# Kernel optimization log

Hardware: AMD Instinct MI355X
Metric: run time of the kernel (lower is better)

Reference implementation:

```python
import jax, jax.numpy as jnp
import numpy as np
from jax import lax

COCO_80_TO_91 = [1,2,3,4,5,6,7,8,9,10,11,13,14,15,16,17,18,19,20,21,22,23,24,25,27,28,31,32,33,34,35,36,37,38,39,40,41,42,43,44,46,47,48,49,50,51,52,53,54,55,56,57,58,59,60,61,62,63,64,65,67,70,72,73,74,75,76,77,78,79,80,81,82,84,85,86,87,88,89,90]

CONF = 0.25      # self.confidence
IOU_THR = 0.7    # ultralytics NMS default
TOPK = 1000      # candidate cap before NMS
MAX_DET = 300    # ultralytics max_det default
MAX_WH = 7680.0  # per-class offset trick
IMG_SZ = 640.0   # yolov8 letterboxed input size


def setup_inputs() -> dict:
    key = jax.random.key(0)
    preds = jax.random.uniform(key, (32, 84, 8400), dtype=jnp.float32)
    return {"preds": preds}


def _nms_single(boxes, scores):
    """Greedy NMS on score-descending boxes [K,4] (class-offset xyxy). Returns keep mask [K]."""
    K = boxes.shape[0]
    area = (boxes[:, 2] - boxes[:, 0]) * (boxes[:, 3] - boxes[:, 1])  # [K]
    lt = jnp.maximum(boxes[:, None, :2], boxes[None, :, :2])          # [K,K,2]
    rb = jnp.minimum(boxes[:, None, 2:], boxes[None, :, 2:])
    wh = jnp.clip(rb - lt, 0.0)
    inter = wh[..., 0] * wh[..., 1]
    iou = inter / (area[:, None] + area[None, :] - inter + 1e-7)       # [K,K]
    idx = jnp.arange(K)
    sup = (iou > IOU_THR) & (idx[None, :] > idx[:, None])              # i suppresses later j

    def body(i, keep):
        return jnp.where(keep[i], keep & ~sup[i], keep)

    return lax.fori_loop(0, K, body, jnp.ones((K,), dtype=bool))


def reference(preds):
    # preds: [B, 84, N] -> [B, N, 84]
    p = jnp.transpose(preds, (0, 2, 1))
    box_xywh = p[..., :4] * IMG_SZ           # xywh in pixels on 640x640 canvas
    cls = p[..., 4:]                          # [B, N, 80]
    scores = jnp.max(cls, axis=-1)            # best-class confidence
    labels = jnp.argmax(cls, axis=-1)         # 0..79
    xy, wh = box_xywh[..., :2], box_xywh[..., 2:]
    xyxy = jnp.concatenate([xy - wh * 0.5, xy + wh * 0.5], axis=-1)  # decode

    # confidence filter + top-K candidate selection (score-descending)
    s_masked = jnp.where(scores > CONF, scores, -1.0)
    top_s, top_i = lax.top_k(s_masked, TOPK)                          # [B,TOPK]
    top_b = jnp.take_along_axis(xyxy, top_i[..., None], axis=1)      # [B,TOPK,4]
    top_l = jnp.take_along_axis(labels, top_i, axis=1)               # [B,TOPK]

    # per-class NMS via class offset
    off_b = top_b + (top_l.astype(top_b.dtype) * MAX_WH)[..., None]
    keep = jax.vmap(_nms_single)(off_b, top_s) & (top_s > CONF)

    # select final max_det detections, zero-pad invalid slots
    fin_s = jnp.where(keep, top_s, -1.0)
    out_s, out_i = lax.top_k(fin_s, MAX_DET)                          # [B,MAX_DET]
    out_b = jnp.take_along_axis(top_b, out_i[..., None], axis=1)
    out_l = jnp.take_along_axis(top_l, out_i, axis=1)
    valid = out_s > CONF
    boxes = jnp.where(valid[..., None], out_b, 0.0)
    scores_out = jnp.where(valid, out_s, 0.0)
    mapped = jnp.asarray(COCO_80_TO_91, dtype=jnp.int64)[out_l]       # COCO 80 -> 91 ids
    labels_out = jnp.where(valid, mapped, 0)
    return boxes, scores_out, labels_out
```

## Files before the change

kernel.cpp:

```cpp
#include <hip/hip_runtime.h>
#include <stdint.h>

typedef unsigned long long u64;
typedef unsigned int u32;

#define BATCH 32
#define NCH 84
#define NA 8400
#define NCLS 80
#define TOPK 1000
#define MAXDET 300
#define CONF 0.25f
#define IOU_T 0.7f
#define MAX_WH 7680.0f
#define IMG_SZ 640.0f
#define NT 1024
#define KPT 9
#define NCOPY 8
#define HPAD 260
#define DTILE 256

__device__ __constant__ float coco_map_f[NCLS] = {
    1,2,3,4,5,6,7,8,9,10,11,13,14,15,16,17,18,19,20,21,22,23,24,25,27,28,
    31,32,33,34,35,36,37,38,39,40,41,42,43,44,46,47,48,49,50,51,52,53,54,
    55,56,57,58,59,60,61,62,63,64,65,67,70,72,73,74,75,76,77,78,79,80,81,
    82,84,85,86,87,88,89,90};

__device__ inline u64 shflx64(u64 v, int m) {
    int lo = __shfl_xor((int)(u32)(v & 0xFFFFFFFFull), m, 64);
    int hi = __shfl_xor((int)(u32)(v >> 32), m, 64);
    return ((u64)(u32)hi << 32) | (u32)lo;
}

__global__ __launch_bounds__(256)
void decode_kernel(const float* __restrict__ preds,
                   u64* __restrict__ keys,
                   float4* __restrict__ boxes) {
    const int b = blockIdx.y;
    const int a_base = blockIdx.x * DTILE;
    const int t = threadIdx.x;
    const int a = a_base + t;
    const float* p = preds + (size_t)b * NCH * NA;

    __shared__ float stage[16][DTILE];

    float bx = 0.f, by = 0.f, bw = 0.f, bh = 0.f;
    float best = -1.0f;
    int bl = 0;

    for (int chunk = 0; chunk < 6; ++chunk) {
        const int r0 = chunk * 16;
        const int nr = (chunk == 5) ? 4 : 16;
        if (chunk) __syncthreads();
        for (int i = 0; i < nr / 4; ++i) {
            int idx = i * 256 + t;
            int rl = idx >> 6;
            int c4 = (idx & 63) * 4;
            int col = a_base + c4;
            float4 v = (col < NA) ? *(const float4*)(p + (size_t)(r0 + rl) * NA + col)
                                  : make_float4(0.f, 0.f, 0.f, 0.f);
            *(float4*)&stage[rl][c4] = v;
        }
        __syncthreads();
        if (chunk == 0) {
            bx = stage[0][t]; by = stage[1][t];
            bw = stage[2][t]; bh = stage[3][t];
            best = stage[4][t]; bl = 0;
            for (int r = 5; r < 16; ++r) {
                float v = stage[r][t];
                int c = r - 4;
                bl = (v > best) ? c : bl;  best = fmaxf(v, best);
            }
        } else {
            for (int r = 0; r < nr; ++r) {
                float v = stage[r][t];
                int c = r0 + r - 4;
                bl = (v > best) ? c : bl;  best = fmaxf(v, best);
            }
        }
    }

    if (a < NA) {
        float fx = bx * IMG_SZ, fy = by * IMG_SZ;
        float fw = bw * IMG_SZ, fh = bh * IMG_SZ;
        float hw = fw * 0.5f, hh = fh * 0.5f;
        boxes[(size_t)b * NA + a] = make_float4(fx - hw, fy - hh, fx + hw, fy + hh);
        float s = (best > CONF) ? best : -1.0f;
        u32 fb = __float_as_uint(s);
        u32 u = (fb & 0x80000000u) ? ~fb : (fb | 0x80000000u);
        keys[(size_t)b * NA + a] =
            ((u64)u << 21) | ((u64)(16383 - a) << 7) | (u64)bl;
    }
}

__global__ __launch_bounds__(NT)
void fused_kernel(const u64* __restrict__ keys,
                  const float4* __restrict__ boxes,
                  float* __restrict__ out) {
    const int b = blockIdx.x;
    const int t = threadIdx.x;
    const int lane = t & 63, wid = t >> 6;

    __shared__ union {
        struct {
            u64 sk[2][NT];
            int hist[NCOPY * HPAD];
        } a;
        struct {
            u64 cmask2[NCLS][16];
        } bb;
        struct {
            float4 obox[NT];
            float  area[NT];
            unsigned short ranks[NCLS][64];
            int    cnt[NCLS];
            unsigned char cls[NT];
            unsigned char keep[NT];
        } c;
    } u_s;
    __shared__ int selB, selK, hselS, smax, scnt, cnt_s;
    __shared__ int wsum[16], woff[16], ktot_s;

    u64 kreg[KPT];
    const u64* kb = keys + (size_t)b * NA;
    int nk = 0;
    for (int i = t; i < NA; i += NT) kreg[nk++] = kb[i];

    u64 P = 0ull;
    int kk = TOPK;
    int nsel = 0;
    for (int d = 6; d >= 0; --d) {
        __syncthreads();
        if (t == 0) { smax = -1; scnt = 0; }
        __syncthreads();
        u64 hmask = (~0ull) << (8 * (d + 1));
        int dig[KPT];
        int mymax = -1;
#pragma unroll
        for (int i = 0; i < KPT; ++i) {
            bool act = (i < nk) && (((kreg[i] ^ P) & hmask) == 0ull);
            dig[i] = act ? (int)((kreg[i] >> (8 * d)) & 255) : -1;
            mymax = max(mymax, dig[i]);
        }
#pragma unroll
        for (int off = 32; off; off >>= 1)
            mymax = max(mymax, __shfl_down(mymax, off, 64));
        if (lane == 0) atomicMax(&smax, mymax);
        __syncthreads();
        int maxb = smax;
        int myc = 0;
#pragma unroll
        for (int i = 0; i < KPT; ++i) myc += (dig[i] == maxb) ? 1 : 0;
#pragma unroll
        for (int off = 32; off; off >>= 1) myc += __shfl_down(myc, off, 64);
        if (lane == 0) atomicAdd(&scnt, myc);
        __syncthreads();
        int cm = scnt;
        if (cm >= kk) {
            P |= ((u64)maxb) << (8 * d);
            nsel = TOPK - kk + cm;
            if (nsel <= NT) break;
            continue;
        }
        for (int i = t; i < NCOPY * HPAD; i += NT) u_s.a.hist[i] = 0;
        __syncthreads();
        int* myh = u_s.a.hist + (wid & (NCOPY - 1)) * HPAD;
#pragma unroll
        for (int i = 0; i < KPT; ++i)
            if (dig[i] >= 0) atomicAdd(&myh[dig[i]], 1);
        __syncthreads();
        if (t < 64) {
            int h0 = 0, h1 = 0, h2 = 0, h3 = 0;
            for (int c = 0; c < NCOPY; ++c) {
                const int* hp = u_s.a.hist + c * HPAD + 4 * t;
                h0 += hp[0]; h1 += hp[1]; h2 += hp[2]; h3 += hp[3];
            }
            int s = h0 + h1 + h2 + h3;
            int S = s;
            #pragma unroll
            for (int off = 1; off < 64; off <<= 1) {
                int o = __shfl_down(S, off, 64);
                if (t + off < 64) S += o;
            }
            int Snext = S - s;
            int c3 = Snext + h3, c2 = c3 + h2, c1 = c2 + h1, c0 = c1 + h0;
            int cand = -1, above = 0;
            if (c0 >= kk) {
                if      (c3 >= kk) { cand = 4 * t + 3; above = Snext; }
                else if (c2 >= kk) { cand = 4 * t + 2; above = c3; }
                else if (c1 >= kk) { cand = 4 * t + 1; above = c2; }
                else               { cand = 4 * t;     above = c1; }
            }
            int pc = (cand < 0) ? 0 : (((cand + 1) << 16) | (kk - above));
            #pragma unroll
            for (int off = 32; off; off >>= 1)
                pc = max(pc, __shfl_down(pc, off, 64));
            pc = __shfl(pc, 0, 64);
            int B = (pc >> 16) - 1;
            if (t == (B >> 2)) {
                int m4 = B & 3;
                selB = B;
                selK = pc & 0xFFFF;
                hselS = (m4 == 0) ? h0 : (m4 == 1) ? h1 : (m4 == 2) ? h2 : h3;
            }
        }
        __syncthreads();
        P |= ((u64)selB) << (8 * d);
        kk = selK;
        nsel = TOPK - kk + hselS;
        if (nsel <= NT) break;
    }

    __syncthreads();
    if (t == 0) cnt_s = 0;
    __syncthreads();
    for (int i = 0; i < KPT; ++i) {
        bool p = (i < nk) && (kreg[i] >= P);
        u64 m = __ballot(p);
        int base = 0;
        if (lane == 0) base = atomicAdd(&cnt_s, (int)__popcll(m));
        base = __shfl(base, 0, 64);
        if (p) u_s.a.sk[0][base + (int)__popcll(m & ((1ull << lane) - 1ull))] = kreg[i];
    }
    if (t < NT - nsel) u_s.a.sk[0][nsel + t] = 0ull;
    __syncthreads();

    u64 myk = u_s.a.sk[0][t];
    int buf = 1;
    for (int size = 2; size <= NT; size <<= 1) {
        bool up = ((t & size) == 0);
        for (int stride = size >> 1; stride; stride >>= 1) {
            u64 pk;
            if (stride >= 64) {
                u_s.a.sk[buf][t] = myk;
                __syncthreads();
                pk = u_s.a.sk[buf][t ^ stride];
                buf ^= 1;
            } else {
                pk = shflx64(myk, stride);
            }
            bool tlow = ((t & stride) == 0);
            u64 mn = (myk < pk) ? myk : pk;
            u64 mx = (myk < pk) ? pk : myk;
            myk = up ? (tlow ? mx : mn) : (tlow ? mn : mx);
        }
    }

    __syncthreads();
    for (int i = t; i < NCLS * 16; i += NT) ((u64*)u_s.bb.cmask2)[i] = 0ull;
    __syncthreads();

    int my_L = 0;
    float sj = -1.0f;
    float4 bx = make_float4(0.f, 0.f, 0.f, 0.f);
    if (t < TOPK) {
        int my_a = 16383 - (int)((myk >> 7) & 16383ull);
        my_L = (int)(myk & 127ull);
        bx = boxes[(size_t)b * NA + my_a];
        u32 u = (u32)(myk >> 21);
        u32 fb = (u & 0x80000000u) ? (u ^ 0x80000000u) : ~u;
        sj = __uint_as_float(fb);
        atomicOr(&u_s.bb.cmask2[my_L][t >> 6], 1ull << (t & 63));
    }
    __syncthreads();
    int r = 0, cntreg = 0;
    if (t < TOPK) {
        int w = t >> 6;
        r = __popcll(u_s.bb.cmask2[my_L][w] & ((1ull << (t & 63)) - 1ull));
        for (int q = 0; q < w; ++q) r += __popcll(u_s.bb.cmask2[my_L][q]);
    }
    if (t < NCLS) {
#pragma unroll
        for (int q = 0; q < 16; ++q) cntreg += __popcll(u_s.bb.cmask2[t][q]);
    }
    __syncthreads();

    float off = (float)my_L * MAX_WH;
    float ox0 = bx.x + off, oy0 = bx.y + off, ox1 = bx.z + off, oy1 = bx.w + off;
    float ar = (ox1 - ox0) * (oy1 - oy0);
    if (t < TOPK) {
        u_s.c.obox[t] = make_float4(ox0, oy0, ox1, oy1);
        u_s.c.area[t] = ar;
        u_s.c.cls[t]  = (unsigned char)my_L;
        if (r < 64) u_s.c.ranks[my_L][r] = (unsigned short)t;
    } else {
        u_s.c.cls[t] = 255;
    }
    u_s.c.keep[t] = 0;
    if (t < NCLS) u_s.c.cnt[t] = cntreg;
    __syncthreads();

    for (int cc = wid; cc < NCLS; cc += 16) {
        int n = u_s.c.cnt[cc];
        if (n == 0) continue;
        if (n <= 64) {
            float4 bbx = make_float4(0.f, 0.f, 0.f, 0.f);
            float aa = 0.f;
            int rk = 0;
            if (lane < n) {
                rk  = u_s.c.ranks[cc][lane];
                bbx = u_s.c.obox[rk];
                aa  = u_s.c.area[rk];
            }
            u64 colm = 0ull;
            for (int i = 0; i < n; ++i) {
                float hx0 = __shfl(bbx.x, i, 64);
                float hy0 = __shfl(bbx.y, i, 64);
                float hx1 = __shfl(bbx.z, i, 64);
                float hy1 = __shfl(bbx.w, i, 64);
                float ha  = __shfl(aa, i, 64);
                float lx = fmaxf(hx0, bbx.x), ly = fmaxf(hy0, bbx.y);
                float rx = fminf(hx1, bbx.z), ry = fminf(hy1, bbx.w);
                float w = fmaxf(rx - lx, 0.0f);
                float h = fmaxf(ry - ly, 0.0f);
                float inter = w * h;
                float denom = ha + aa;
                denom = denom - inter;
                denom = denom + 1e-7f;
                bool s = (lane > i) && (lane < n) && (inter / denom > IOU_T);
                colm |= ((u64)s) << i;
            }
            u64 alive = (n >= 64) ? ~0ull : ((1ull << n) - 1ull);
            for (int i = 0; i < n; ++i) {
                if (!((alive >> i) & 1ull)) continue;
                alive &= ~__ballot((colm >> i) & 1ull);
            }
            if (lane < n) u_s.c.keep[rk] = (unsigned char)((alive >> lane) & 1ull);
        } else if (lane == 0) {
            u64 aliveW[16];
            for (int q = 0; q < 16; ++q) aliveW[q] = ~0ull;
            for (int i = 0; i < TOPK; ++i) {
                if (u_s.c.cls[i] != (unsigned char)cc) continue;
                if (!((aliveW[i >> 6] >> (i & 63)) & 1ull)) continue;
                float4 bi = u_s.c.obox[i];
                float ai = u_s.c.area[i];
                for (int j = i + 1; j < TOPK; ++j) {
                    if (u_s.c.cls[j] != (unsigned char)cc) continue;
                    if (!((aliveW[j >> 6] >> (j & 63)) & 1ull)) continue;
                    float4 bj = u_s.c.obox[j];
                    float lx = fmaxf(bi.x, bj.x), ly = fmaxf(bi.y, bj.y);
                    float rx = fminf(bi.z, bj.z), ry = fminf(bi.w, bj.w);
                    float w = fmaxf(rx - lx, 0.0f);
                    float h = fmaxf(ry - ly, 0.0f);
                    float inter = w * h;
                    float denom = ai + u_s.c.area[j];
                    denom = denom - inter;
                    denom = denom + 1e-7f;
                    if (inter / denom > IOU_T) aliveW[j >> 6] &= ~(1ull << (j & 63));
                }
            }
            for (int i = 0; i < TOPK; ++i)
                if (u_s.c.cls[i] == (unsigned char)cc)
                    u_s.c.keep[i] = (unsigned char)((aliveW[i >> 6] >> (i & 63)) & 1ull);
        }
    }
    __syncthreads();

    bool valid = (t < TOPK) && u_s.c.keep[t] && (sj > CONF);
    u64 m = __ballot(valid);
    if (lane == 0) wsum[wid] = (int)__popcll(m);
    __syncthreads();
    if (wid == 0) {
        int v = (lane < 16) ? wsum[lane] : 0;
        #pragma unroll
        for (int o = 1; o < 16; o <<= 1) {
            int x = __shfl_up(v, o, 64);
            if (lane >= o) v += x;
        }
        if (lane < 16) woff[lane] = v - wsum[lane];
        if (lane == 15) ktot_s = v;
    }
    __syncthreads();
    int ktot = ktot_s;
    int rank = woff[wid] + (int)__popcll(m & ((1ull << lane) - 1ull));

    float* out_boxes = out;
    float* out_scores = out + (size_t)BATCH * MAXDET * 4;
    float* out_labels = out + (size_t)BATCH * MAXDET * 5;
    if (valid && rank < MAXDET) {
        float* ob = out_boxes + ((size_t)b * MAXDET + rank) * 4;
        ob[0] = bx.x; ob[1] = bx.y; ob[2] = bx.z; ob[3] = bx.w;
        out_scores[(size_t)b * MAXDET + rank] = sj;
        out_labels[(size_t)b * MAXDET + rank] = coco_map_f[my_L];
    }
    if (t < MAXDET && t >= ktot) {
        float* ob = out_boxes + ((size_t)b * MAXDET + t) * 4;
        ob[0] = 0.0f; ob[1] = 0.0f; ob[2] = 0.0f; ob[3] = 0.0f;
        out_scores[(size_t)b * MAXDET + t] = 0.0f;
        out_labels[(size_t)b * MAXDET + t] = 0.0f;
    }
}

extern "C" void kernel_launch(void* const* d_in, const int* in_sizes, int n_in,
                              void* d_out, int out_size, void* d_ws, size_t ws_size,
                              hipStream_t stream) {
    const float* preds = (const float*)d_in[0];
    char* ws = (char*)d_ws;
    size_t off = 0;
    auto alloc = [&](size_t bytes) { char* p = ws + off; off += (bytes + 255) & ~(size_t)255; return p; };

    u64* keys     = (u64*)    alloc((size_t)BATCH * NA * 8);
    float4* boxes = (float4*) alloc((size_t)BATCH * NA * 16);
    float* out = (float*)d_out;

    dim3 dgrid((NA + DTILE - 1) / DTILE, BATCH);
    decode_kernel<<<dgrid, 256, 0, stream>>>(preds, keys, boxes);
    fused_kernel<<<BATCH, NT, 0, stream>>>(keys, boxes, out);
}
```

Before: 189.4 us.

## Split fused select/NMS kernel, skip low radix digits, use per-wave decode staging

The decode kernel now has each wave stage its own 64 columns in shared memory and sync with s_waitcnt instead of block-wide barriers. The radix select only walks the four score digits, since the low key bits are anchor index and label and never matter for score ties at the top-k boundary. The single fused kernel is split into a select+sort kernel that writes sorted keys, boxes, per-class ranks and counts to global memory, and an NMS/epilogue kernel that reads them back. The split cuts shared-memory use per kernel but adds a launch and global round-trips, and the large-class fallback now reads from global memory.

Result: faster. 184.1 us (-2.8%).

```diff
diff --git a/kernel.cpp b/kernel.cpp
--- a/kernel.cpp
+++ b/kernel.cpp
@@ -37,47 +37,50 @@
                    u64* __restrict__ keys,
                    float4* __restrict__ boxes) {
     const int b = blockIdx.y;
-    const int a_base = blockIdx.x * DTILE;
     const int t = threadIdx.x;
-    const int a = a_base + t;
+    const int w = t >> 6, l = t & 63;
+    const int wa = blockIdx.x * DTILE + w * 64;
+    const int a = wa + l;
     const float* p = preds + (size_t)b * NCH * NA;
 
-    __shared__ float stage[16][DTILE];
+    __shared__ float stage[4][16][64];
 
     float bx = 0.f, by = 0.f, bw = 0.f, bh = 0.f;
     float best = -1.0f;
     int bl = 0;
 
+    const int rsel = l >> 4;
+    const int c4 = (l & 15) * 4;
+    const int col = wa + c4;
+
     for (int chunk = 0; chunk < 6; ++chunk) {
         const int r0 = chunk * 16;
+        const int nq = (chunk == 5) ? 1 : 4;
+        for (int i = 0; i < nq; ++i) {
+            int row = r0 + i * 4 + rsel;
+            float4 v = (col < NA) ? *(const float4*)(p + (size_t)row * NA + col)
+                                  : make_float4(0.f, 0.f, 0.f, 0.f);
+            *(float4*)&stage[w][i * 4 + rsel][c4] = v;
+        }
+        __builtin_amdgcn_s_waitcnt(0xc07f);
         const int nr = (chunk == 5) ? 4 : 16;
-        if (chunk) __syncthreads();
-        for (int i = 0; i < nr / 4; ++i) {
-            int idx = i * 256 + t;
-            int rl = idx >> 6;
-            int c4 = (idx & 63) * 4;
-            int col = a_base + c4;
-            float4 v = (col < NA) ? *(const float4*)(p + (size_t)(r0 + rl) * NA + col)
-                                  : make_float4(0.f, 0.f, 0.f, 0.f);
-            *(float4*)&stage[rl][c4] = v;
-        }
-        __syncthreads();
         if (chunk == 0) {
-            bx = stage[0][t]; by = stage[1][t];
-            bw = stage[2][t]; bh = stage[3][t];
-            best = stage[4][t]; bl = 0;
+            bx = stage[w][0][l]; by = stage[w][1][l];
+            bw = stage[w][2][l]; bh = stage[w][3][l];
+            best = stage[w][4][l]; bl = 0;
             for (int r = 5; r < 16; ++r) {
-                float v = stage[r][t];
+                float v = stage[w][r][l];
                 int c = r - 4;
                 bl = (v > best) ? c : bl;  best = fmaxf(v, best);
             }
         } else {
             for (int r = 0; r < nr; ++r) {
-                float v = stage[r][t];
+                float v = stage[w][r][l];
                 int c = r0 + r - 4;
                 bl = (v > best) ? c : bl;  best = fmaxf(v, best);
             }
         }
+        __builtin_amdgcn_s_waitcnt(0xc07f);
     }
 
     if (a < NA) {
@@ -94,9 +97,12 @@
 }
 
 __global__ __launch_bounds__(NT)
-void fused_kernel(const u64* __restrict__ keys,
-                  const float4* __restrict__ boxes,
-                  float* __restrict__ out) {
+void select_sort_kernel(const u64* __restrict__ keys,
+                        const float4* __restrict__ boxes,
+                        u64* __restrict__ sortedk,
+                        float4* __restrict__ gbox,
+                        unsigned short* __restrict__ grank,
+                        int* __restrict__ gccnt) {
     const int b = blockIdx.x;
     const int t = threadIdx.x;
     const int lane = t & 63, wid = t >> 6;
@@ -109,17 +115,8 @@
         struct {
             u64 cmask2[NCLS][16];
         } bb;
-        struct {
-            float4 obox[NT];
-            float  area[NT];
-            unsigned short ranks[NCLS][64];
-            int    cnt[NCLS];
-            unsigned char cls[NT];
-            unsigned char keep[NT];
-        } c;
     } u_s;
     __shared__ int selB, selK, hselS, smax, scnt, cnt_s;
-    __shared__ int wsum[16], woff[16], ktot_s;
 
     u64 kreg[KPT];
     const u64* kb = keys + (size_t)b * NA;
@@ -129,17 +126,18 @@
     u64 P = 0ull;
     int kk = TOPK;
     int nsel = 0;
-    for (int d = 6; d >= 0; --d) {
+    for (int d = 3; d >= 0; --d) {
+        const int sh = 21 + 8 * d;
         __syncthreads();
         if (t == 0) { smax = -1; scnt = 0; }
         __syncthreads();
-        u64 hmask = (~0ull) << (8 * (d + 1));
+        u64 hmask = (~0ull) << (sh + 8);
         int dig[KPT];
         int mymax = -1;
 #pragma unroll
         for (int i = 0; i < KPT; ++i) {
             bool act = (i < nk) && (((kreg[i] ^ P) & hmask) == 0ull);
-            dig[i] = act ? (int)((kreg[i] >> (8 * d)) & 255) : -1;
+            dig[i] = act ? (int)((kreg[i] >> sh) & 255) : -1;
             mymax = max(mymax, dig[i]);
         }
 #pragma unroll
@@ -157,7 +155,7 @@
         __syncthreads();
         int cm = scnt;
         if (cm >= kk) {
-            P |= ((u64)maxb) << (8 * d);
+            P |= ((u64)maxb) << sh;
             nsel = TOPK - kk + cm;
             if (nsel <= NT) break;
             continue;
@@ -205,7 +203,7 @@
             }
         }
         __syncthreads();
-        P |= ((u64)selB) << (8 * d);
+        P |= ((u64)selB) << sh;
         kk = selK;
         nsel = TOPK - kk + hselS;
         if (nsel <= NT) break;
@@ -220,7 +218,10 @@
         int base = 0;
         if (lane == 0) base = atomicAdd(&cnt_s, (int)__popcll(m));
         base = __shfl(base, 0, 64);
-        if (p) u_s.a.sk[0][base + (int)__popcll(m & ((1ull << lane) - 1ull))] = kreg[i];
+        if (p) {
+            int pos = base + (int)__popcll(m & ((1ull << lane) - 1ull));
+            if (pos < NT) u_s.a.sk[0][pos] = kreg[i];
+        }
     }
     if (t < NT - nsel) u_s.a.sk[0][nsel + t] = 0ull;
     __syncthreads();
@@ -245,62 +246,73 @@
             myk = up ? (tlow ? mx : mn) : (tlow ? mn : mx);
         }
     }
+    sortedk[(size_t)b * NT + t] = myk;
 
     __syncthreads();
     for (int i = t; i < NCLS * 16; i += NT) ((u64*)u_s.bb.cmask2)[i] = 0ull;
     __syncthreads();
 
     int my_L = 0;
-    float sj = -1.0f;
     float4 bx = make_float4(0.f, 0.f, 0.f, 0.f);
     if (t < TOPK) {
         int my_a = 16383 - (int)((myk >> 7) & 16383ull);
         my_L = (int)(myk & 127ull);
         bx = boxes[(size_t)b * NA + my_a];
-        u32 u = (u32)(myk >> 21);
-        u32 fb = (u & 0x80000000u) ? (u ^ 0x80000000u) : ~u;
-        sj = __uint_as_float(fb);
         atomicOr(&u_s.bb.cmask2[my_L][t >> 6], 1ull << (t & 63));
     }
     __syncthreads();
-    int r = 0, cntreg = 0;
     if (t < TOPK) {
         int w = t >> 6;
-        r = __popcll(u_s.bb.cmask2[my_L][w] & ((1ull << (t & 63)) - 1ull));
+        int r = __popcll(u_s.bb.cmask2[my_L][w] & ((1ull << (t & 63)) - 1ull));
         for (int q = 0; q < w; ++q) r += __popcll(u_s.bb.cmask2[my_L][q]);
+        gbox[(size_t)b * NT + t] = bx;
+        if (r < 64) grank[((size_t)b * NCLS + my_L) * 64 + r] = (unsigned short)t;
     }
     if (t < NCLS) {
-#pragma unroll
-        for (int q = 0; q < 16; ++q) cntreg += __popcll(u_s.bb.cmask2[t][q]);
-    }
-    __syncthreads();
-
-    float off = (float)my_L * MAX_WH;
-    float ox0 = bx.x + off, oy0 = bx.y + off, ox1 = bx.z + off, oy1 = bx.w + off;
-    float ar = (ox1 - ox0) * (oy1 - oy0);
-    if (t < TOPK) {
-        u_s.c.obox[t] = make_float4(ox0, oy0, ox1, oy1);
-        u_s.c.area[t] = ar;
-        u_s.c.cls[t]  = (unsigned char)my_L;
-        if (r < 64) u_s.c.ranks[my_L][r] = (unsigned short)t;
-    } else {
-        u_s.c.cls[t] = 255;
-    }
-    u_s.c.keep[t] = 0;
-    if (t < NCLS) u_s.c.cnt[t] = cntreg;
-    __syncthreads();
-
-    for (int cc = wid; cc < NCLS; cc += 16) {
-        int n = u_s.c.cnt[cc];
+        int s = 0;
+#pragma unroll
+        for (int q = 0; q < 16; ++q) s += __popcll(u_s.bb.cmask2[t][q]);
+        gccnt[(size_t)b * NCLS + t] = s;
+    }
+}
+
+__global__ __launch_bounds__(NT)
+void nms_epi_kernel(const u64* __restrict__ sortedk,
+                    const float4* __restrict__ gbox,
+                    const unsigned short* __restrict__ grank,
+                    const int* __restrict__ gccnt,
+                    float* __restrict__ out) {
+    const int b = blockIdx.x;
+    const int t = threadIdx.x;
+    const int lane = t & 63, wid = t >> 6;
+
+    __shared__ unsigned char keep[NT];
+    __shared__ int wsum[16], woff[16], ktot_s;
+
+    keep[t] = 0;
+
+    int cnts[5];
+#pragma unroll
+    for (int j = 0; j < 5; ++j)
+        cnts[j] = gccnt[(size_t)b * NCLS + wid + 16 * j];
+
+    u64 myk = sortedk[(size_t)b * NT + t];
+    __syncthreads();
+
+    for (int j = 0; j < 5; ++j) {
+        const int cc = wid + 16 * j;
+        const int n = cnts[j];
         if (n == 0) continue;
         if (n <= 64) {
             float4 bbx = make_float4(0.f, 0.f, 0.f, 0.f);
             float aa = 0.f;
             int rk = 0;
             if (lane < n) {
-                rk  = u_s.c.ranks[cc][lane];
-                bbx = u_s.c.obox[rk];
-                aa  = u_s.c.area[rk];
+                rk = grank[((size_t)b * NCLS + cc) * 64 + lane];
+                float4 g = gbox[(size_t)b * NT + rk];
+                float off = (float)cc * MAX_WH;
+                bbx = make_float4(g.x + off, g.y + off, g.z + off, g.w + off);
+                aa = (bbx.z - bbx.x) * (bbx.w - bbx.y);
             }
             u64 colm = 0ull;
             for (int i = 0; i < n; ++i) {
@@ -325,38 +337,53 @@
                 if (!((alive >> i) & 1ull)) continue;
                 alive &= ~__ballot((colm >> i) & 1ull);
             }
-            if (lane < n) u_s.c.keep[rk] = (unsigned char)((alive >> lane) & 1ull);
+            if (lane < n) keep[rk] = (unsigned char)((alive >> lane) & 1ull);
         } else if (lane == 0) {
+            const u64* skb = sortedk + (size_t)b * NT;
+            const float4* gb = gbox + (size_t)b * NT;
+            const float off = (float)cc * MAX_WH;
             u64 aliveW[16];
             for (int q = 0; q < 16; ++q) aliveW[q] = ~0ull;
             for (int i = 0; i < TOPK; ++i) {
-                if (u_s.c.cls[i] != (unsigned char)cc) continue;
+                if ((int)(skb[i] & 127ull) != cc) continue;
                 if (!((aliveW[i >> 6] >> (i & 63)) & 1ull)) continue;
-                float4 bi = u_s.c.obox[i];
-                float ai = u_s.c.area[i];
-                for (int j = i + 1; j < TOPK; ++j) {
-                    if (u_s.c.cls[j] != (unsigned char)cc) continue;
-                    if (!((aliveW[j >> 6] >> (j & 63)) & 1ull)) continue;
-                    float4 bj = u_s.c.obox[j];
-                    float lx = fmaxf(bi.x, bj.x), ly = fmaxf(bi.y, bj.y);
-                    float rx = fminf(bi.z, bj.z), ry = fminf(bi.w, bj.w);
-                    float w = fmaxf(rx - lx, 0.0f);
-                    float h = fmaxf(ry - ly, 0.0f);
-                    float inter = w * h;
-                    float denom = ai + u_s.c.area[j];
+                float4 g = gb[i];
+                float ix0 = g.x + off, iy0 = g.y + off;
+                float ix1 = g.z + off, iy1 = g.w + off;
+                float ai = (ix1 - ix0) * (iy1 - iy0);
+                for (int jj = i + 1; jj < TOPK; ++jj) {
+                    if ((int)(skb[jj] & 127ull) != cc) continue;
+                    if (!((aliveW[jj >> 6] >> (jj & 63)) & 1ull)) continue;
+                    float4 h = gb[jj];
+                    float jx0 = h.x + off, jy0 = h.y + off;
+                    float jx1 = h.z + off, jy1 = h.w + off;
+                    float aj = (jx1 - jx0) * (jy1 - jy0);
+                    float lx = fmaxf(ix0, jx0), ly = fmaxf(iy0, jy0);
+                    float rx = fminf(ix1, jx1), ry = fminf(iy1, jy1);
+                    float ww = fmaxf(rx - lx, 0.0f);
+                    float hh = fmaxf(ry - ly, 0.0f);
+                    float inter = ww * hh;
+                    float denom = ai + aj;
                     denom = denom - inter;
                     denom = denom + 1e-7f;
-                    if (inter / denom > IOU_T) aliveW[j >> 6] &= ~(1ull << (j & 63));
+                    if (inter / denom > IOU_T) aliveW[jj >> 6] &= ~(1ull << (jj & 63));
                 }
             }
             for (int i = 0; i < TOPK; ++i)
-                if (u_s.c.cls[i] == (unsigned char)cc)
-                    u_s.c.keep[i] = (unsigned char)((aliveW[i >> 6] >> (i & 63)) & 1ull);
-        }
-    }
-    __syncthreads();
-
-    bool valid = (t < TOPK) && u_s.c.keep[t] && (sj > CONF);
+                if ((int)(skb[i] & 127ull) == cc)
+                    keep[i] = (unsigned char)((aliveW[i >> 6] >> (i & 63)) & 1ull);
+        }
+    }
+    __syncthreads();
+
+    float sj = 0.0f;
+    bool valid = false;
+    if (t < TOPK) {
+        u32 u = (u32)(myk >> 21);
+        u32 fb = (u & 0x80000000u) ? (u ^ 0x80000000u) : ~u;
+        sj = __uint_as_float(fb);
+        valid = keep[t] && (sj > CONF);
+    }
     u64 m = __ballot(valid);
     if (lane == 0) wsum[wid] = (int)__popcll(m);
     __syncthreads();
@@ -378,10 +405,11 @@
     float* out_scores = out + (size_t)BATCH * MAXDET * 4;
     float* out_labels = out + (size_t)BATCH * MAXDET * 5;
     if (valid && rank < MAXDET) {
+        float4 bx = gbox[(size_t)b * NT + t];
         float* ob = out_boxes + ((size_t)b * MAXDET + rank) * 4;
         ob[0] = bx.x; ob[1] = bx.y; ob[2] = bx.z; ob[3] = bx.w;
         out_scores[(size_t)b * MAXDET + rank] = sj;
-        out_labels[(size_t)b * MAXDET + rank] = coco_map_f[my_L];
+        out_labels[(size_t)b * MAXDET + rank] = coco_map_f[(int)(myk & 127ull)];
     }
     if (t < MAXDET && t >= ktot) {
         float* ob = out_boxes + ((size_t)b * MAXDET + t) * 4;
@@ -399,11 +427,17 @@
     size_t off = 0;
     auto alloc = [&](size_t bytes) { char* p = ws + off; off += (bytes + 255) & ~(size_t)255; return p; };
 
-    u64* keys     = (u64*)    alloc((size_t)BATCH * NA * 8);
-    float4* boxes = (float4*) alloc((size_t)BATCH * NA * 16);
+    u64* keys            = (u64*)           alloc((size_t)BATCH * NA * 8);
+    float4* boxes        = (float4*)        alloc((size_t)BATCH * NA * 16);
+    u64* sortedk         = (u64*)           alloc((size_t)BATCH * NT * 8);
+    float4* gbox         = (float4*)        alloc((size_t)BATCH * NT * 16);
+    unsigned short* grank= (unsigned short*)alloc((size_t)BATCH * NCLS * 64 * 2);
+    int* gccnt           = (int*)           alloc((size_t)BATCH * NCLS * 4);
     float* out = (float*)d_out;
 
     dim3 dgrid((NA + DTILE - 1) / DTILE, BATCH);
     decode_kernel<<<dgrid, 256, 0, stream>>>(preds, keys, boxes);
-    fused_kernel<<<BATCH, NT, 0, stream>>>(keys, boxes, out);
+    select_sort_kernel<<<BATCH, NT, 0, stream>>>(keys, boxes, sortedk,
+                                                 gbox, grank, gccnt);
+    nms_epi_kernel<<<BATCH, NT, 0, stream>>>(sortedk, gbox, grank, gccnt, out);
 }
```

## Use per-wave staging in decode and shorten radix select to score digits

Applied to the files above, without the earlier changes.

The decode kernel now stages its rows per wavefront, so each wave loads and reads only its own slice. This replaces the block-wide __syncthreads with s_waitcnt. The top-K radix select now starts at the score bits of the packed key, running four 8-bit passes from bit 21 upward instead of seven passes from bit 0. Key loading is fully unrolled with zero-fill, and a bound check guards the candidate scatter. Dropping the low index bits from the select could change which candidates are kept when scores tie, and relying on waitcnt without a barrier assumes LDS accesses within a wave are ordered.

New measurement: 176.3 us. 6.9% less time.

```diff
diff --git a/kernel.cpp b/kernel.cpp
--- a/kernel.cpp
+++ b/kernel.cpp
@@ -37,47 +37,50 @@
                    u64* __restrict__ keys,
                    float4* __restrict__ boxes) {
     const int b = blockIdx.y;
-    const int a_base = blockIdx.x * DTILE;
     const int t = threadIdx.x;
-    const int a = a_base + t;
+    const int w = t >> 6, l = t & 63;
+    const int wa = blockIdx.x * DTILE + w * 64;
+    const int a = wa + l;
     const float* p = preds + (size_t)b * NCH * NA;
 
-    __shared__ float stage[16][DTILE];
+    __shared__ float stage[4][16][64];
 
     float bx = 0.f, by = 0.f, bw = 0.f, bh = 0.f;
     float best = -1.0f;
     int bl = 0;
 
+    const int rsel = l >> 4;
+    const int c4 = (l & 15) * 4;
+    const int col = wa + c4;
+
     for (int chunk = 0; chunk < 6; ++chunk) {
         const int r0 = chunk * 16;
+        const int nq = (chunk == 5) ? 1 : 4;
+        for (int i = 0; i < nq; ++i) {
+            int row = r0 + i * 4 + rsel;
+            float4 v = (col < NA) ? *(const float4*)(p + (size_t)row * NA + col)
+                                  : make_float4(0.f, 0.f, 0.f, 0.f);
+            *(float4*)&stage[w][i * 4 + rsel][c4] = v;
+        }
+        __builtin_amdgcn_s_waitcnt(0xc07f);
         const int nr = (chunk == 5) ? 4 : 16;
-        if (chunk) __syncthreads();
-        for (int i = 0; i < nr / 4; ++i) {
-            int idx = i * 256 + t;
-            int rl = idx >> 6;
-            int c4 = (idx & 63) * 4;
-            int col = a_base + c4;
-            float4 v = (col < NA) ? *(const float4*)(p + (size_t)(r0 + rl) * NA + col)
-                                  : make_float4(0.f, 0.f, 0.f, 0.f);
-            *(float4*)&stage[rl][c4] = v;
-        }
-        __syncthreads();
         if (chunk == 0) {
-            bx = stage[0][t]; by = stage[1][t];
-            bw = stage[2][t]; bh = stage[3][t];
-            best = stage[4][t]; bl = 0;
+            bx = stage[w][0][l]; by = stage[w][1][l];
+            bw = stage[w][2][l]; bh = stage[w][3][l];
+            best = stage[w][4][l]; bl = 0;
             for (int r = 5; r < 16; ++r) {
-                float v = stage[r][t];
+                float v = stage[w][r][l];
                 int c = r - 4;
                 bl = (v > best) ? c : bl;  best = fmaxf(v, best);
             }
         } else {
             for (int r = 0; r < nr; ++r) {
-                float v = stage[r][t];
+                float v = stage[w][r][l];
                 int c = r0 + r - 4;
                 bl = (v > best) ? c : bl;  best = fmaxf(v, best);
             }
         }
+        __builtin_amdgcn_s_waitcnt(0xc07f);
     }
 
     if (a < NA) {
@@ -93,7 +96,7 @@
     }
 }
 
-__global__ __launch_bounds__(NT)
+__global__ __launch_bounds__(NT, 4)
 void fused_kernel(const u64* __restrict__ keys,
                   const float4* __restrict__ boxes,
                   float* __restrict__ out) {
@@ -123,24 +126,28 @@
 
     u64 kreg[KPT];
     const u64* kb = keys + (size_t)b * NA;
-    int nk = 0;
-    for (int i = t; i < NA; i += NT) kreg[nk++] = kb[i];
+#pragma unroll
+    for (int j = 0; j < KPT; ++j) {
+        int i = t + j * NT;
+        kreg[j] = (i < NA) ? kb[i] : 0ull;
+    }
 
     u64 P = 0ull;
     int kk = TOPK;
     int nsel = 0;
-    for (int d = 6; d >= 0; --d) {
+    for (int d = 3; d >= 0; --d) {
+        const int sh = 21 + 8 * d;
         __syncthreads();
         if (t == 0) { smax = -1; scnt = 0; }
         __syncthreads();
-        u64 hmask = (~0ull) << (8 * (d + 1));
+        u64 hmask = (~0ull) << (sh + 8);
         int dig[KPT];
         int mymax = -1;
 #pragma unroll
-        for (int i = 0; i < KPT; ++i) {
-            bool act = (i < nk) && (((kreg[i] ^ P) & hmask) == 0ull);
-            dig[i] = act ? (int)((kreg[i] >> (8 * d)) & 255) : -1;
-            mymax = max(mymax, dig[i]);
+        for (int j = 0; j < KPT; ++j) {
+            bool act = (((kreg[j] ^ P) & hmask) == 0ull) && (kreg[j] != 0ull);
+            dig[j] = act ? (int)((kreg[j] >> sh) & 255) : -1;
+            mymax = max(mymax, dig[j]);
         }
 #pragma unroll
         for (int off = 32; off; off >>= 1)
@@ -150,14 +157,14 @@
         int maxb = smax;
         int myc = 0;
 #pragma unroll
-        for (int i = 0; i < KPT; ++i) myc += (dig[i] == maxb) ? 1 : 0;
+        for (int j = 0; j < KPT; ++j) myc += (dig[j] == maxb) ? 1 : 0;
 #pragma unroll
         for (int off = 32; off; off >>= 1) myc += __shfl_down(myc, off, 64);
         if (lane == 0) atomicAdd(&scnt, myc);
         __syncthreads();
         int cm = scnt;
         if (cm >= kk) {
-            P |= ((u64)maxb) << (8 * d);
+            P |= ((u64)maxb) << sh;
             nsel = TOPK - kk + cm;
             if (nsel <= NT) break;
             continue;
@@ -166,8 +173,8 @@
         __syncthreads();
         int* myh = u_s.a.hist + (wid & (NCOPY - 1)) * HPAD;
 #pragma unroll
-        for (int i = 0; i < KPT; ++i)
-            if (dig[i] >= 0) atomicAdd(&myh[dig[i]], 1);
+        for (int j = 0; j < KPT; ++j)
+            if (dig[j] >= 0) atomicAdd(&myh[dig[j]], 1);
         __syncthreads();
         if (t < 64) {
             int h0 = 0, h1 = 0, h2 = 0, h3 = 0;
@@ -205,7 +212,7 @@
             }
         }
         __syncthreads();
-        P |= ((u64)selB) << (8 * d);
+        P |= ((u64)selB) << sh;
         kk = selK;
         nsel = TOPK - kk + hselS;
         if (nsel <= NT) break;
@@ -214,13 +221,17 @@
     __syncthreads();
     if (t == 0) cnt_s = 0;
     __syncthreads();
-    for (int i = 0; i < KPT; ++i) {
-        bool p = (i < nk) && (kreg[i] >= P);
+#pragma unroll
+    for (int j = 0; j < KPT; ++j) {
+        bool p = (kreg[j] >= P);
         u64 m = __ballot(p);
         int base = 0;
         if (lane == 0) base = atomicAdd(&cnt_s, (int)__popcll(m));
         base = __shfl(base, 0, 64);
-        if (p) u_s.a.sk[0][base + (int)__popcll(m & ((1ull << lane) - 1ull))] = kreg[i];
+        if (p) {
+            int pos = base + (int)__popcll(m & ((1ull << lane) - 1ull));
+            if (pos < NT) u_s.a.sk[0][pos] = kreg[j];
+        }
     }
     if (t < NT - nsel) u_s.a.sk[0][nsel + t] = 0ull;
     __syncthreads();
@@ -290,8 +301,9 @@
     if (t < NCLS) u_s.c.cnt[t] = cntreg;
     __syncthreads();
 
-    for (int cc = wid; cc < NCLS; cc += 16) {
-        int n = u_s.c.cnt[cc];
+    for (int jc = 0; jc < 5; ++jc) {
+        const int cc = wid + 16 * jc;
+        const int n = u_s.c.cnt[cc];
         if (n == 0) continue;
         if (n <= 64) {
             float4 bbx = make_float4(0.f, 0.f, 0.f, 0.f);
@@ -334,19 +346,19 @@
                 if (!((aliveW[i >> 6] >> (i & 63)) & 1ull)) continue;
                 float4 bi = u_s.c.obox[i];
                 float ai = u_s.c.area[i];
-                for (int j = i + 1; j < TOPK; ++j) {
-                    if (u_s.c.cls[j] != (unsigned char)cc) continue;
-                    if (!((aliveW[j >> 6] >> (j & 63)) & 1ull)) continue;
-                    float4 bj = u_s.c.obox[j];
+                for (int jj = i + 1; jj < TOPK; ++jj) {
+                    if (u_s.c.cls[jj] != (unsigned char)cc) continue;
+                    if (!((aliveW[jj >> 6] >> (jj & 63)) & 1ull)) continue;
+                    float4 bj = u_s.c.obox[jj];
                     float lx = fmaxf(bi.x, bj.x), ly = fmaxf(bi.y, bj.y);
                     float rx = fminf(bi.z, bj.z), ry = fminf(bi.w, bj.w);
                     float w = fmaxf(rx - lx, 0.0f);
                     float h = fmaxf(ry - ly, 0.0f);
                     float inter = w * h;
-                    float denom = ai + u_s.c.area[j];
+                    float denom = ai + u_s.c.area[jj];
                     denom = denom - inter;
                     denom = denom + 1e-7f;
-                    if (inter / denom > IOU_T) aliveW[j >> 6] &= ~(1ull << (j & 63));
+                    if (inter / denom > IOU_T) aliveW[jj >> 6] &= ~(1ull << (jj & 63));
                 }
             }
             for (int i = 0; i < TOPK; ++i)
```
